# Kernel optimization log

Measured on AMD Instinct MI355X. Metric: run time of the kernel, lower is better.

## Reference

```python
import jax, jax.numpy as jnp
import numpy as np

B, S, D = 4, 2048, 256
H = 8
HD = D // H
FF = 1024
LEN_M1 = 513


def _layer_norm(x, gamma, beta, eps=1e-5):
    m = jnp.mean(x, axis=-1, keepdims=True)
    v = jnp.var(x, axis=-1, keepdims=True)
    return (x - m) * jax.lax.rsqrt(v + eps) * gamma + beta


def setup_inputs() -> dict:
    key = jax.random.key(0)
    ks = jax.random.split(key, 16)
    s = 0.02  # init scale for weights
    return {
        "src": jax.random.normal(ks[0], (B, S, D), dtype=jnp.float32),
        "Wq": jax.random.normal(ks[1], (D, D), dtype=jnp.float32) * s,
        "bq": jnp.zeros((D,), dtype=jnp.float32),
        "Wk": jax.random.normal(ks[2], (D, D), dtype=jnp.float32) * s,
        "bk": jnp.zeros((D,), dtype=jnp.float32),
        "Wv": jax.random.normal(ks[3], (D, D), dtype=jnp.float32) * s,
        "bv": jnp.zeros((D,), dtype=jnp.float32),
        "Wo": jax.random.normal(ks[4], (D, D), dtype=jnp.float32) * s,
        "bo": jnp.zeros((D,), dtype=jnp.float32),
        "W1": jax.random.normal(ks[5], (FF, D), dtype=jnp.float32) * s,
        "b1": jnp.zeros((FF,), dtype=jnp.float32),
        "W2": jax.random.normal(ks[6], (D, FF), dtype=jnp.float32) * s,
        "b2": jnp.zeros((D,), dtype=jnp.float32),
        "g1": jnp.ones((D,), dtype=jnp.float32),
        "be1": jnp.zeros((D,), dtype=jnp.float32),
        "g2": jnp.ones((D,), dtype=jnp.float32),
        "be2": jnp.zeros((D,), dtype=jnp.float32),
        "len_m1": LEN_M1,
    }


def reference(src, Wq, bq, Wk, bk, Wv, bv, Wo, bo, W1, b1, W2, b2, g1, be1, g2, be2, len_m1):
    Bb, Ss, Dd = src.shape
    hd = Dd // H
    # projections (torch Linear: x @ W.T + b), split heads -> [B,H,S,hd]
    q = (src @ Wq.T + bq).reshape(Bb, Ss, H, hd).transpose(0, 2, 1, 3)
    k = (src @ Wk.T + bk).reshape(Bb, Ss, H, hd).transpose(0, 2, 1, 3)
    v = (src @ Wv.T + bv).reshape(Bb, Ss, H, hd).transpose(0, 2, 1, 3)
    scores = jnp.einsum("bhqd,bhkd->bhqk", q, k) / np.sqrt(hd).astype(np.float32)
    # causal mask + global prefix block: masked where j > i OR (i < len_m1 and j >= len_m1)
    i = jnp.arange(Ss)[:, None]
    j = jnp.arange(Ss)[None, :]
    mask = (j > i) | ((i < len_m1) & (j >= len_m1))
    scores = jnp.where(mask, -jnp.inf, scores)
    attn = jax.nn.softmax(scores, axis=-1)
    ao = jnp.einsum("bhqk,bhkd->bhqd", attn, v).transpose(0, 2, 1, 3).reshape(Bb, Ss, Dd)
    src2 = _layer_norm(src + (ao @ Wo.T + bo), g1, be1)
    ff = jax.nn.gelu(src2 @ W1.T + b1, approximate=False) @ W2.T + b2
    return _layer_norm(src2 + ff, g2, be2)
```

## Files before the change

kernel.cpp:

```cpp
#include <hip/hip_runtime.h>
#include <math.h>

#define NB 4
#define NS 2048
#define ND 256
#define NH 8
#define NHD 32
#define NFF 1024
#define NM (NB*NS)
#define KPAD 40
#define VSP 72
#define VTP 72
#define AS 264
#define QSCALE 0.2550181657f

typedef __attribute__((ext_vector_type(4))) short short4v;
typedef __attribute__((ext_vector_type(8))) short short8v;
typedef __attribute__((ext_vector_type(4))) float f32x4;
typedef unsigned short us;

__device__ __forceinline__ us f2bf(float f){
  union { float f; unsigned u; } c; c.f = f;
  unsigned u = c.u + 0x7fffu + ((c.u >> 16) & 1u);
  return (us)(u >> 16);
}

__device__ __forceinline__ float wsum(float v){
  #pragma unroll
  for(int o=32;o>0;o>>=1) v += __shfl_xor(v,o);
  return v;
}

__global__ __launch_bounds__(256) void prep_kernel(
    const float* __restrict__ src,
    const float* __restrict__ Wq, const float* __restrict__ Wk, const float* __restrict__ Wv,
    const float* __restrict__ Wo, const float* __restrict__ W1, const float* __restrict__ W2,
    const float* __restrict__ bq,
    us* __restrict__ X, us* __restrict__ Wqkvb, us* __restrict__ Wob,
    us* __restrict__ W1b, us* __restrict__ W2b, float* __restrict__ bqs){
  unsigned bid = blockIdx.x;
  if (bid == 1408){ bqs[threadIdx.x] = bq[threadIdx.x]*QSCALE; return; }
  unsigned u = bid*256u + threadIdx.x;
  const float* sp; us* dp; float sc = 1.f;
  if (u < 262144u){ sp = src + (size_t)u*8; dp = X + (size_t)u*8; }
  else {
    unsigned v = u - 262144u;
    if      (v <  8192u){ sp = Wq + (size_t)v*8;            dp = Wqkvb + (size_t)v*8;            sc = QSCALE; }
    else if (v < 16384u){ sp = Wk + (size_t)(v- 8192u)*8;   dp = Wqkvb + 65536 + (size_t)(v- 8192u)*8; }
    else if (v < 24576u){ sp = Wv + (size_t)(v-16384u)*8;   dp = Wqkvb + 131072 + (size_t)(v-16384u)*8; }
    else if (v < 32768u){ sp = Wo + (size_t)(v-24576u)*8;   dp = Wob + (size_t)(v-24576u)*8; }
    else if (v < 65536u){ sp = W1 + (size_t)(v-32768u)*8;   dp = W1b + (size_t)(v-32768u)*8; }
    else               { sp = W2 + (size_t)(v-65536u)*8;    dp = W2b + (size_t)(v-65536u)*8; }
  }
  float4 a = *(const float4*)sp, b = *(const float4*)(sp+4);
  short8v o;
  o[0]=(short)f2bf(a.x*sc); o[1]=(short)f2bf(a.y*sc); o[2]=(short)f2bf(a.z*sc); o[3]=(short)f2bf(a.w*sc);
  o[4]=(short)f2bf(b.x*sc); o[5]=(short)f2bf(b.y*sc); o[6]=(short)f2bf(b.z*sc); o[7]=(short)f2bf(b.w*sc);
  *(short8v*)dp = o;
}

template<int KTOT, int EPI>
__global__ __launch_bounds__(256) void gemm_kernel(
    const us* __restrict__ A, const us* __restrict__ W,
    const float* __restrict__ bias0, const float* __restrict__ bias1, const float* __restrict__ bias2,
    us* __restrict__ outb, us* __restrict__ outv){
  __shared__ us Asl[64*AS];
  const int t = threadIdx.x, l = t&63, wv = t>>6;
  const int lx = l&15, lw = l>>4;
  const int m0 = blockIdx.y*64;
  const int n0 = blockIdx.x*128 + wv*32;

  f32x4 acc[4][2];
  #pragma unroll
  for(int mb=0;mb<4;mb++)
    #pragma unroll
    for(int nb=0;nb<2;nb++) acc[mb][nb] = (f32x4){0.f,0.f,0.f,0.f};

  for (int kc = 0; kc < KTOT; kc += 256){
    __syncthreads();
    #pragma unroll
    for (int it=0; it<8; it++){
      int idx = it*256 + t;
      int r = idx>>5, c = idx&31;
      *(short8v*)&Asl[r*AS + c*8] = *(const short8v*)(A + (size_t)(m0+r)*KTOT + kc + c*8);
    }
    __syncthreads();
    short8v bf[2][8];
    #pragma unroll
    for (int nb=0; nb<2; nb++)
      #pragma unroll
      for (int ks=0; ks<8; ks++)
        bf[nb][ks] = *(const short8v*)(W + (size_t)(n0 + nb*16 + lx)*KTOT + kc + ks*32 + 8*lw);
    #pragma unroll
    for (int ks=0; ks<8; ks++){
      short8v af[4];
      #pragma unroll
      for (int mb=0; mb<4; mb++)
        af[mb] = *(const short8v*)&Asl[(mb*16+lx)*AS + ks*32 + 8*lw];
      #pragma unroll
      for (int mb=0; mb<4; mb++){
        acc[mb][0] = __builtin_amdgcn_mfma_f32_16x16x32_bf16(af[mb], bf[0][ks], acc[mb][0], 0,0,0);
        acc[mb][1] = __builtin_amdgcn_mfma_f32_16x16x32_bf16(af[mb], bf[1][ks], acc[mb][1], 0,0,0);
      }
    }
  }
  const int mr0 = m0 + 4*lw;
  #pragma unroll
  for (int nb=0; nb<2; nb++){
    int n = n0 + nb*16 + lx;
    if (EPI == 0){
      int seg = n >> 8, nn = n & 255;
      const float* bp = (seg==0) ? bias0 : (seg==1) ? bias1 : bias2;
      float bb = bp[nn];
      if (seg < 2){
        us* op = outb + (size_t)seg*((size_t)NM*ND) + nn;
        #pragma unroll
        for (int mb=0; mb<4; mb++)
          #pragma unroll
          for (int r=0; r<4; r++)
            op[(size_t)(mr0 + mb*16 + r)*ND] = f2bf(acc[mb][nb][r] + bb);
      } else {
        int hh = nn >> 5, dd = nn & 31;
        int bidx = mr0 >> 11;
        int s0 = mr0 & 2047;
        us* vp = outv + (((size_t)bidx*NH + hh)*NHD + dd)*NS;
        #pragma unroll
        for (int mb=0; mb<4; mb++){
          short4v v4;
          #pragma unroll
          for (int r=0; r<4; r++) v4[r] = (short)f2bf(acc[mb][nb][r] + bb);
          *(short4v*)(vp + s0 + mb*16) = v4;
        }
      }
    } else {
      float bb = bias0[n];
      #pragma unroll
      for (int mb=0; mb<4; mb++)
        #pragma unroll
        for (int r=0; r<4; r++){
          float x = acc[mb][nb][r] + bb;
          float g = 0.5f*x*(1.f + erff(x*0.70710678118654752f));
          outb[(size_t)(mr0 + mb*16 + r)*NFF + n] = f2bf(g);
        }
    }
  }
}

template<int KTOT>
__global__ __launch_bounds__(256) void gemm2_kernel(
    const us* __restrict__ A, const us* __restrict__ W,
    const float* __restrict__ bias, const float* __restrict__ resid,
    float* __restrict__ outf){
  __shared__ us Asl[32*AS];
  const int t = threadIdx.x, l = t&63, wv = t>>6;
  const int lx = l&15, lw = l>>4;
  const int m0 = blockIdx.y*32;
  const int n0 = blockIdx.x*128 + wv*32;

  f32x4 acc[2][2];
  #pragma unroll
  for(int mb=0;mb<2;mb++)
    #pragma unroll
    for(int nb=0;nb<2;nb++) acc[mb][nb] = (f32x4){0.f,0.f,0.f,0.f};

  for (int kc = 0; kc < KTOT; kc += 256){
    __syncthreads();
    #pragma unroll
    for (int it=0; it<4; it++){
      int idx = it*256 + t;
      int r = idx>>5, c = idx&31;
      *(short8v*)&Asl[r*AS + c*8] = *(const short8v*)(A + (size_t)(m0+r)*KTOT + kc + c*8);
    }
    __syncthreads();
    short8v bf[2][8];
    #pragma unroll
    for (int nb=0; nb<2; nb++)
      #pragma unroll
      for (int ks=0; ks<8; ks++)
        bf[nb][ks] = *(const short8v*)(W + (size_t)(n0 + nb*16 + lx)*KTOT + kc + ks*32 + 8*lw);
    #pragma unroll
    for (int ks=0; ks<8; ks++){
      short8v af[2];
      #pragma unroll
      for (int mb=0; mb<2; mb++)
        af[mb] = *(const short8v*)&Asl[(mb*16+lx)*AS + ks*32 + 8*lw];
      #pragma unroll
      for (int mb=0; mb<2; mb++){
        acc[mb][0] = __builtin_amdgcn_mfma_f32_16x16x32_bf16(af[mb], bf[0][ks], acc[mb][0], 0,0,0);
        acc[mb][1] = __builtin_amdgcn_mfma_f32_16x16x32_bf16(af[mb], bf[1][ks], acc[mb][1], 0,0,0);
      }
    }
  }
  const int mr0 = m0 + 4*lw;
  #pragma unroll
  for (int nb=0; nb<2; nb++){
    int n = n0 + nb*16 + lx;
    float bb = bias[n];
    #pragma unroll
    for (int mb=0; mb<2; mb++)
      #pragma unroll
      for (int r=0; r<4; r++){
        size_t off = (size_t)(mr0 + mb*16 + r)*ND + n;
        outf[off] = acc[mb][nb][r] + bb + resid[off];
      }
  }
}

__global__ __launch_bounds__(256) void ln_kernel(
    const float* __restrict__ Xin, const float* __restrict__ g, const float* __restrict__ be,
    us* __restrict__ outb, float* __restrict__ outf){
  const int t = threadIdx.x, lane = t&63, wv = t>>6;
  const int m0 = blockIdx.x*16;
  #pragma unroll
  for(int rr=0; rr<4; rr++){
    int r = m0 + wv*4 + rr;
    const float* xr = Xin + (size_t)r*ND;
    float x[4]; float s=0.f,q=0.f;
    #pragma unroll
    for(int k=0;k<4;k++){ x[k]=xr[lane+64*k]; s+=x[k]; q+=x[k]*x[k]; }
    s = wsum(s); q = wsum(q);
    float mean = s*(1.f/ND), var = q*(1.f/ND)-mean*mean;
    float rstd = rsqrtf(var+1e-5f);
    #pragma unroll
    for(int k=0;k<4;k++){
      int col = lane+64*k;
      float y = (x[k]-mean)*rstd*g[col] + be[col];
      if (outf) outf[(size_t)r*ND+col] = y;
      if (outb) outb[(size_t)r*ND+col] = f2bf(y);
    }
  }
}

template<bool MASK>
__device__ __forceinline__ void attn_tile(
    const us* __restrict__ Kl, const us* __restrict__ Vl,
    const short8v qf, const int lx, const int lw, const int jt, const int qg,
    f32x4& acc0, f32x4& acc1, float& lsum){
  f32x4 s4[4];
  #pragma unroll
  for (int kb=0; kb<4; kb++){
    short8v kf = *(const short8v*)(Kl + (kb*16 + lx)*KPAD + 8*lw);
    f32x4 z = {0.f,0.f,0.f,0.f};
    s4[kb] = __builtin_amdgcn_mfma_f32_16x16x32_bf16(kf, qf, z, 0,0,0);
  }
  float p[16];
  #pragma unroll
  for (int kb=0; kb<4; kb++)
    #pragma unroll
    for (int r=0; r<4; r++){
      float x = exp2f(s4[kb][r]);
      if (MASK) x = ((jt + 16*kb + 4*lw + r) > qg) ? 0.f : x;
      p[kb*4+r] = x;
    }
  {
    float a0=p[0]+p[1],   a1=p[2]+p[3],   a2=p[4]+p[5],   a3=p[6]+p[7];
    float a4=p[8]+p[9],   a5=p[10]+p[11], a6=p[12]+p[13], a7=p[14]+p[15];
    float b0=a0+a1, b1=a2+a3, b2=a4+a5, b3=a6+a7;
    lsum += (b0+b1) + (b2+b3);
  }
  #pragma unroll
  for (int c=0; c<2; c++){
    unsigned w0,w1,w2,w3;
    asm("v_cvt_pk_bf16_f32 %0, %1, %2" : "=v"(w0) : "v"(p[8*c+0]), "v"(p[8*c+1]));
    asm("v_cvt_pk_bf16_f32 %0, %1, %2" : "=v"(w1) : "v"(p[8*c+2]), "v"(p[8*c+3]));
    asm("v_cvt_pk_bf16_f32 %0, %1, %2" : "=v"(w2) : "v"(p[8*c+4]), "v"(p[8*c+5]));
    asm("v_cvt_pk_bf16_f32 %0, %1, %2" : "=v"(w3) : "v"(p[8*c+6]), "v"(p[8*c+7]));
    union { unsigned u[4]; short8v v; } pu;
    pu.u[0]=w0; pu.u[1]=w1; pu.u[2]=w2; pu.u[3]=w3;
    short8v pf = pu.v;
    short8v aL = *(const short8v*)(Vl + (size_t)( lx    )*VSP + 32*c + 8*lw);
    short8v aH = *(const short8v*)(Vl + (size_t)(16+lx  )*VSP + 32*c + 8*lw);
    acc0 = __builtin_amdgcn_mfma_f32_16x16x32_bf16(aL, pf, acc0, 0,0,0);
    acc1 = __builtin_amdgcn_mfma_f32_16x16x32_bf16(aH, pf, acc1, 0,0,0);
  }
}

__global__ __launch_bounds__(256) void attn_kernel(
    const us* __restrict__ Q, const us* __restrict__ K,
    const us* __restrict__ Vt, us* __restrict__ AO){
  __shared__ us Klds[2][64*KPAD];
  __shared__ us Vs[2][32*VSP];
  __shared__ us Ex[4][16*VTP];

  const int t = threadIdx.x, l = t & 63, wv = t >> 6;
  const int lx = l & 15, lw = l >> 4;
  const int bid = blockIdx.x;
  const int qtile = 31 - (bid >> 5);
  const int bh = bid & 31;
  const int b = bh >> 3, h = bh & 7;
  const int qbase = qtile*64 + wv*16;
  const int qg = qbase + lx;

  const us* Qg = Q + ((size_t)b*NS)*ND + h*NHD;
  const us* Kg = K + ((size_t)b*NS)*ND + h*NHD;
  const us* Vg = Vt + (size_t)bh*NHD*NS;

  short8v qf = *(const short8v*)(Qg + (size_t)(qbase + lx)*ND + 8*lw);

  f32x4 acc0 = {0.f,0.f,0.f,0.f}, acc1 = {0.f,0.f,0.f,0.f};
  float lsum = 0.f;

  const int kr = t >> 2, kp = t & 3;
  const int vd = t >> 3, vp = t & 7;
  const int vS0 = 32*(vp>>2) + 16*(vp&1) + 4*((vp>>1)&1);
  const int jmax = qtile*64;

  {
    short8v k0 = *(const short8v*)(Kg + (size_t)kr*ND + kp*8);
    short8v v0 = *(const short8v*)(Vg + (size_t)vd*NS + vp*8);
    *(short8v*)&Klds[0][kr*KPAD + kp*8] = k0;
    short4v lo = {v0[0],v0[1],v0[2],v0[3]}, hi = {v0[4],v0[5],v0[6],v0[7]};
    *(short4v*)&Vs[0][vd*VSP + vS0]     = lo;
    *(short4v*)&Vs[0][vd*VSP + vS0 + 8] = hi;
  }
  __syncthreads();

  int cur = 0;
  for (int jt = 0; jt < jmax; jt += 64){
    short8v kn = *(const short8v*)(Kg + (size_t)(jt + 64 + kr)*ND + kp*8);
    short8v vn = *(const short8v*)(Vg + (size_t)vd*NS + (jt + 64) + vp*8);
    attn_tile<false>(&Klds[cur][0], &Vs[cur][0], qf, lx, lw, jt, qg, acc0, acc1, lsum);
    *(short8v*)&Klds[cur^1][kr*KPAD + kp*8] = kn;
    short4v lo = {vn[0],vn[1],vn[2],vn[3]}, hi = {vn[4],vn[5],vn[6],vn[7]};
    *(short4v*)&Vs[cur^1][vd*VSP + vS0]     = lo;
    *(short4v*)&Vs[cur^1][vd*VSP + vS0 + 8] = hi;
    __syncthreads();
    cur ^= 1;
  }
  attn_tile<true>(&Klds[cur][0], &Vs[cur][0], qf, lx, lw, jmax, qg, acc0, acc1, lsum);

  float lt = lsum + __shfl_xor(lsum, 16);
  lt += __shfl_xor(lt, 32);
  float inv = 1.f / lt;
  float* ol = (float*)&Ex[wv][0];
  #pragma unroll
  for (int r=0;r<4;r++){
    ol[lx*36 +      4*lw + r] = acc0[r]*inv;
    ol[lx*36 + 16 + 4*lw + r] = acc1[r]*inv;
  }
  int rr = l >> 2, cc = l & 3;
  const float* op8 = &ol[rr*36 + cc*8];
  short8v o8;
  #pragma unroll
  for (int j=0;j<8;j++) o8[j] = (short)f2bf(op8[j]);
  *(short8v*)(AO + ((size_t)(b*NS + qbase + rr))*ND + h*NHD + cc*8) = o8;
}

extern "C" void kernel_launch(void* const* d_in, const int* in_sizes, int n_in,
                              void* d_out, int out_size, void* d_ws, size_t ws_size,
                              hipStream_t stream){
  const float* src = (const float*)d_in[0];
  const float* Wq  = (const float*)d_in[1];
  const float* bq  = (const float*)d_in[2];
  const float* Wk  = (const float*)d_in[3];
  const float* bk  = (const float*)d_in[4];
  const float* Wv  = (const float*)d_in[5];
  const float* bv  = (const float*)d_in[6];
  const float* Wo  = (const float*)d_in[7];
  const float* bo  = (const float*)d_in[8];
  const float* W1  = (const float*)d_in[9];
  const float* b1  = (const float*)d_in[10];
  const float* W2  = (const float*)d_in[11];
  const float* b2  = (const float*)d_in[12];
  const float* g1  = (const float*)d_in[13];
  const float* be1 = (const float*)d_in[14];
  const float* g2  = (const float*)d_in[15];
  const float* be2 = (const float*)d_in[16];

  const size_t MB = 1048576;
  unsigned char* w8 = (unsigned char*)d_ws;
  us* X     = (us*)(w8 + 0);
  us* Qb    = (us*)(w8 + 4*MB);
  us* Kb    = (us*)(w8 + 8*MB);
  us* Vtg   = (us*)(w8 + 12*MB);
  us* AO    = (us*)(w8 + 16*MB);
  us* S2b   = (us*)(w8 + 20*MB);
  us* FF    = (us*)(w8 + 24*MB);
  us* Wqkvb = (us*)(w8 + 40*MB);
  us* Wob   = (us*)(w8 + 40*MB + 384*1024);
  us* W1b   = (us*)(w8 + 40*MB + 512*1024);
  us* W2b   = (us*)(w8 + 40*MB + 1024*1024);
  float* bqs   = (float*)(w8 + 40*MB + 1536*1024);
  float* S2pre = (float*)(w8 + 42*MB);
  float* S2f   = (float*)(w8 + 50*MB);
  float* Ypre  = (float*)(w8 + 0);
  float* out = (float*)d_out;

  prep_kernel<<<1409, 256, 0, stream>>>(src, Wq,Wk,Wv,Wo,W1,W2, bq,
                                        X, Wqkvb, Wob, W1b, W2b, bqs);
  gemm_kernel<256,0><<<dim3(6,128), 256, 0, stream>>>(X, Wqkvb, bqs, bk, bv, Qb, Vtg);
  attn_kernel<<<1024, 256, 0, stream>>>(Qb, Kb, Vtg, AO);
  gemm2_kernel<256><<<dim3(2,256), 256, 0, stream>>>(AO, Wob, bo, src, S2pre);
  ln_kernel<<<NM/16, 256, 0, stream>>>(S2pre, g1, be1, S2b, S2f);
  gemm_kernel<256,2><<<dim3(8,128), 256, 0, stream>>>(S2b, W1b, b1, nullptr, nullptr, FF, nullptr);
  gemm2_kernel<1024><<<dim3(2,256), 256, 0, stream>>>(FF, W2b, b2, S2f, Ypre);
  ln_kernel<<<NM/16, 256, 0, stream>>>(Ypre, g2, be2, nullptr, out);
}
```

Measured before the change: 111.0 us.

## Fuse input conversion into QKV GEMM and LayerNorm1 into FFN1 GEMM

```diff
diff --git a/kernel.cpp b/kernel.cpp
--- a/kernel.cpp
+++ b/kernel.cpp
@@ -24,6 +24,9 @@
   unsigned u = c.u + 0x7fffu + ((c.u >> 16) & 1u);
   return (us)(u >> 16);
 }
+__device__ __forceinline__ float bf2f(us u){
+  union { unsigned u; float f; } c; c.u = ((unsigned)u) << 16; return c.f;
+}
 
 __device__ __forceinline__ float wsum(float v){
   #pragma unroll
@@ -32,26 +35,21 @@
 }
 
 __global__ __launch_bounds__(256) void prep_kernel(
-    const float* __restrict__ src,
     const float* __restrict__ Wq, const float* __restrict__ Wk, const float* __restrict__ Wv,
     const float* __restrict__ Wo, const float* __restrict__ W1, const float* __restrict__ W2,
     const float* __restrict__ bq,
-    us* __restrict__ X, us* __restrict__ Wqkvb, us* __restrict__ Wob,
+    us* __restrict__ Wqkvb, us* __restrict__ Wob,
     us* __restrict__ W1b, us* __restrict__ W2b, float* __restrict__ bqs){
   unsigned bid = blockIdx.x;
-  if (bid == 1408){ bqs[threadIdx.x] = bq[threadIdx.x]*QSCALE; return; }
-  unsigned u = bid*256u + threadIdx.x;
+  if (bid == 384){ bqs[threadIdx.x] = bq[threadIdx.x]*QSCALE; return; }
+  unsigned v = bid*256u + threadIdx.x;
   const float* sp; us* dp; float sc = 1.f;
-  if (u < 262144u){ sp = src + (size_t)u*8; dp = X + (size_t)u*8; }
-  else {
-    unsigned v = u - 262144u;
-    if      (v <  8192u){ sp = Wq + (size_t)v*8;            dp = Wqkvb + (size_t)v*8;            sc = QSCALE; }
-    else if (v < 16384u){ sp = Wk + (size_t)(v- 8192u)*8;   dp = Wqkvb + 65536 + (size_t)(v- 8192u)*8; }
-    else if (v < 24576u){ sp = Wv + (size_t)(v-16384u)*8;   dp = Wqkvb + 131072 + (size_t)(v-16384u)*8; }
-    else if (v < 32768u){ sp = Wo + (size_t)(v-24576u)*8;   dp = Wob + (size_t)(v-24576u)*8; }
-    else if (v < 65536u){ sp = W1 + (size_t)(v-32768u)*8;   dp = W1b + (size_t)(v-32768u)*8; }
-    else               { sp = W2 + (size_t)(v-65536u)*8;    dp = W2b + (size_t)(v-65536u)*8; }
-  }
+  if      (v <  8192u){ sp = Wq + (size_t)v*8;            dp = Wqkvb + (size_t)v*8;            sc = QSCALE; }
+  else if (v < 16384u){ sp = Wk + (size_t)(v- 8192u)*8;   dp = Wqkvb + 65536 + (size_t)(v- 8192u)*8; }
+  else if (v < 24576u){ sp = Wv + (size_t)(v-16384u)*8;   dp = Wqkvb + 131072 + (size_t)(v-16384u)*8; }
+  else if (v < 32768u){ sp = Wo + (size_t)(v-24576u)*8;   dp = Wob + (size_t)(v-24576u)*8; }
+  else if (v < 65536u){ sp = W1 + (size_t)(v-32768u)*8;   dp = W1b + (size_t)(v-32768u)*8; }
+  else               { sp = W2 + (size_t)(v-65536u)*8;    dp = W2b + (size_t)(v-65536u)*8; }
   float4 a = *(const float4*)sp, b = *(const float4*)(sp+4);
   short8v o;
   o[0]=(short)f2bf(a.x*sc); o[1]=(short)f2bf(a.y*sc); o[2]=(short)f2bf(a.z*sc); o[3]=(short)f2bf(a.w*sc);
@@ -59,11 +57,13 @@
   *(short8v*)dp = o;
 }
 
-template<int KTOT, int EPI>
+template<int KTOT, int EPI, int AF32>
 __global__ __launch_bounds__(256) void gemm_kernel(
-    const us* __restrict__ A, const us* __restrict__ W,
+    const us* __restrict__ A, const float* __restrict__ Af,
+    const us* __restrict__ W,
     const float* __restrict__ bias0, const float* __restrict__ bias1, const float* __restrict__ bias2,
-    us* __restrict__ outb, us* __restrict__ outv){
+    const float* __restrict__ resid, const us* __restrict__ residb,
+    us* __restrict__ outb, us* __restrict__ outv, float* __restrict__ outf){
   __shared__ us Asl[64*AS];
   const int t = threadIdx.x, l = t&63, wv = t>>6;
   const int lx = l&15, lw = l>>4;
@@ -78,11 +78,22 @@
 
   for (int kc = 0; kc < KTOT; kc += 256){
     __syncthreads();
-    #pragma unroll
-    for (int it=0; it<8; it++){
-      int idx = it*256 + t;
-      int r = idx>>5, c = idx&31;
-      *(short8v*)&Asl[r*AS + c*8] = *(const short8v*)(A + (size_t)(m0+r)*KTOT + kc + c*8);
+    if (AF32){
+      #pragma unroll
+      for (int it=0; it<16; it++){
+        int idx = it*256 + t;
+        int r = idx>>6, c = idx&63;
+        float4 v = *(const float4*)(Af + (size_t)(m0+r)*KTOT + kc + c*4);
+        short4v o4 = { (short)f2bf(v.x),(short)f2bf(v.y),(short)f2bf(v.z),(short)f2bf(v.w) };
+        *(short4v*)&Asl[r*AS + c*4] = o4;
+      }
+    } else {
+      #pragma unroll
+      for (int it=0; it<8; it++){
+        int idx = it*256 + t;
+        int r = idx>>5, c = idx&31;
+        *(short8v*)&Asl[r*AS + c*8] = *(const short8v*)(A + (size_t)(m0+r)*KTOT + kc + c*8);
+      }
     }
     __syncthreads();
     short8v bf[2][8];
@@ -132,6 +143,24 @@
           *(short4v*)(vp + s0 + mb*16) = v4;
         }
       }
+    } else if (EPI == 1){
+      float bb = bias0[n];
+      #pragma unroll
+      for (int mb=0; mb<4; mb++)
+        #pragma unroll
+        for (int r=0; r<4; r++){
+          size_t off = (size_t)(mr0 + mb*16 + r)*ND + n;
+          outf[off] = acc[mb][nb][r] + bb + resid[off];
+        }
+    } else if (EPI == 3){
+      float bb = bias0[n];
+      #pragma unroll
+      for (int mb=0; mb<4; mb++)
+        #pragma unroll
+        for (int r=0; r<4; r++){
+          size_t off = (size_t)(mr0 + mb*16 + r)*ND + n;
+          outf[off] = acc[mb][nb][r] + bb + bf2f(residb[off]);
+        }
     } else {
       float bb = bias0[n];
       #pragma unroll
@@ -146,49 +175,58 @@
   }
 }
 
-template<int KTOT>
-__global__ __launch_bounds__(256) void gemm2_kernel(
-    const us* __restrict__ A, const us* __restrict__ W,
-    const float* __restrict__ bias, const float* __restrict__ resid,
-    float* __restrict__ outf){
-  __shared__ us Asl[32*AS];
+__global__ __launch_bounds__(256) void ffn1_ln_kernel(
+    const float* __restrict__ S2pre, const float* __restrict__ g, const float* __restrict__ be,
+    const us* __restrict__ W, const float* __restrict__ bias,
+    us* __restrict__ S2b, us* __restrict__ FF){
+  __shared__ us Asl[64*AS];
   const int t = threadIdx.x, l = t&63, wv = t>>6;
   const int lx = l&15, lw = l>>4;
-  const int m0 = blockIdx.y*32;
+  const int m0 = blockIdx.y*64;
   const int n0 = blockIdx.x*128 + wv*32;
 
-  f32x4 acc[2][2];
-  #pragma unroll
-  for(int mb=0;mb<2;mb++)
+  #pragma unroll
+  for (int rr=0; rr<16; rr++){
+    int rl = wv*16 + rr;
+    const float* xr = S2pre + (size_t)(m0+rl)*ND;
+    float x[4]; float s=0.f,q=0.f;
+    #pragma unroll
+    for (int k=0;k<4;k++){ x[k]=xr[l+64*k]; s+=x[k]; q+=x[k]*x[k]; }
+    s = wsum(s); q = wsum(q);
+    float mean = s*(1.f/ND), var = q*(1.f/ND)-mean*mean;
+    float rstd = rsqrtf(var+1e-5f);
+    #pragma unroll
+    for (int k=0;k<4;k++){
+      int col = l+64*k;
+      us y = f2bf((x[k]-mean)*rstd*g[col] + be[col]);
+      Asl[rl*AS + col] = y;
+      S2b[(size_t)(m0+rl)*ND + col] = y;
+    }
+  }
+  __syncthreads();
+
+  f32x4 acc[4][2];
+  #pragma unroll
+  for(int mb=0;mb<4;mb++)
     #pragma unroll
     for(int nb=0;nb<2;nb++) acc[mb][nb] = (f32x4){0.f,0.f,0.f,0.f};
 
-  for (int kc = 0; kc < KTOT; kc += 256){
-    __syncthreads();
-    #pragma unroll
-    for (int it=0; it<4; it++){
-      int idx = it*256 + t;
-      int r = idx>>5, c = idx&31;
-      *(short8v*)&Asl[r*AS + c*8] = *(const short8v*)(A + (size_t)(m0+r)*KTOT + kc + c*8);
-    }
-    __syncthreads();
-    short8v bf[2][8];
-    #pragma unroll
-    for (int nb=0; nb<2; nb++)
-      #pragma unroll
-      for (int ks=0; ks<8; ks++)
-        bf[nb][ks] = *(const short8v*)(W + (size_t)(n0 + nb*16 + lx)*KTOT + kc + ks*32 + 8*lw);
-    #pragma unroll
-    for (int ks=0; ks<8; ks++){
-      short8v af[2];
-      #pragma unroll
-      for (int mb=0; mb<2; mb++)
-        af[mb] = *(const short8v*)&Asl[(mb*16+lx)*AS + ks*32 + 8*lw];
-      #pragma unroll
-      for (int mb=0; mb<2; mb++){
-        acc[mb][0] = __builtin_amdgcn_mfma_f32_16x16x32_bf16(af[mb], bf[0][ks], acc[mb][0], 0,0,0);
-        acc[mb][1] = __builtin_amdgcn_mfma_f32_16x16x32_bf16(af[mb], bf[1][ks], acc[mb][1], 0,0,0);
-      }
+  short8v bf[2][8];
+  #pragma unroll
+  for (int nb=0; nb<2; nb++)
+    #pragma unroll
+    for (int ks=0; ks<8; ks++)
+      bf[nb][ks] = *(const short8v*)(W + (size_t)(n0 + nb*16 + lx)*ND + ks*32 + 8*lw);
+  #pragma unroll
+  for (int ks=0; ks<8; ks++){
+    short8v af[4];
+    #pragma unroll
+    for (int mb=0; mb<4; mb++)
+      af[mb] = *(const short8v*)&Asl[(mb*16+lx)*AS + ks*32 + 8*lw];
+    #pragma unroll
+    for (int mb=0; mb<4; mb++){
+      acc[mb][0] = __builtin_amdgcn_mfma_f32_16x16x32_bf16(af[mb], bf[0][ks], acc[mb][0], 0,0,0);
+      acc[mb][1] = __builtin_amdgcn_mfma_f32_16x16x32_bf16(af[mb], bf[1][ks], acc[mb][1], 0,0,0);
     }
   }
   const int mr0 = m0 + 4*lw;
@@ -197,18 +235,19 @@
     int n = n0 + nb*16 + lx;
     float bb = bias[n];
     #pragma unroll
-    for (int mb=0; mb<2; mb++)
+    for (int mb=0; mb<4; mb++)
       #pragma unroll
       for (int r=0; r<4; r++){
-        size_t off = (size_t)(mr0 + mb*16 + r)*ND + n;
-        outf[off] = acc[mb][nb][r] + bb + resid[off];
+        float x = acc[mb][nb][r] + bb;
+        float gl = 0.5f*x*(1.f + erff(x*0.70710678118654752f));
+        FF[(size_t)(mr0 + mb*16 + r)*NFF + n] = f2bf(gl);
       }
   }
 }
 
 __global__ __launch_bounds__(256) void ln_kernel(
     const float* __restrict__ Xin, const float* __restrict__ g, const float* __restrict__ be,
-    us* __restrict__ outb, float* __restrict__ outf){
+    float* __restrict__ outf){
   const int t = threadIdx.x, lane = t&63, wv = t>>6;
   const int m0 = blockIdx.x*16;
   #pragma unroll
@@ -224,9 +263,7 @@
     #pragma unroll
     for(int k=0;k<4;k++){
       int col = lane+64*k;
-      float y = (x[k]-mean)*rstd*g[col] + be[col];
-      if (outf) outf[(size_t)r*ND+col] = y;
-      if (outb) outb[(size_t)r*ND+col] = f2bf(y);
+      outf[(size_t)r*ND+col] = (x[k]-mean)*rstd*g[col] + be[col];
     }
   }
 }
@@ -369,7 +406,6 @@
 
   const size_t MB = 1048576;
   unsigned char* w8 = (unsigned char*)d_ws;
-  us* X     = (us*)(w8 + 0);
   us* Qb    = (us*)(w8 + 4*MB);
   us* Kb    = (us*)(w8 + 8*MB);
   us* Vtg   = (us*)(w8 + 12*MB);
@@ -382,17 +418,16 @@
   us* W2b   = (us*)(w8 + 40*MB + 1024*1024);
   float* bqs   = (float*)(w8 + 40*MB + 1536*1024);
   float* S2pre = (float*)(w8 + 42*MB);
-  float* S2f   = (float*)(w8 + 50*MB);
   float* Ypre  = (float*)(w8 + 0);
+  Ypre = (float*)(w8 + 50*MB);
   float* out = (float*)d_out;
 
-  prep_kernel<<<1409, 256, 0, stream>>>(src, Wq,Wk,Wv,Wo,W1,W2, bq,
-                                        X, Wqkvb, Wob, W1b, W2b, bqs);
-  gemm_kernel<256,0><<<dim3(6,128), 256, 0, stream>>>(X, Wqkvb, bqs, bk, bv, Qb, Vtg);
+  prep_kernel<<<385, 256, 0, stream>>>(Wq,Wk,Wv,Wo,W1,W2, bq,
+                                       Wqkvb, Wob, W1b, W2b, bqs);
+  gemm_kernel<256,0,1><<<dim3(6,128), 256, 0, stream>>>(nullptr, src, Wqkvb, bqs, bk, bv, nullptr, nullptr, Qb, Vtg, nullptr);
   attn_kernel<<<1024, 256, 0, stream>>>(Qb, Kb, Vtg, AO);
-  gemm2_kernel<256><<<dim3(2,256), 256, 0, stream>>>(AO, Wob, bo, src, S2pre);
-  ln_kernel<<<NM/16, 256, 0, stream>>>(S2pre, g1, be1, S2b, S2f);
-  gemm_kernel<256,2><<<dim3(8,128), 256, 0, stream>>>(S2b, W1b, b1, nullptr, nullptr, FF, nullptr);
-  gemm2_kernel<1024><<<dim3(2,256), 256, 0, stream>>>(FF, W2b, b2, S2f, Ypre);
-  ln_kernel<<<NM/16, 256, 0, stream>>>(Ypre, g2, be2, nullptr, out);
-}
+  gemm_kernel<256,1,0><<<dim3(2,128), 256, 0, stream>>>(AO, nullptr, Wob, bo, nullptr, nullptr, src, nullptr, nullptr, nullptr, S2pre);
+  ffn1_ln_kernel<<<dim3(8,128), 256, 0, stream>>>(S2pre, g1, be1, W1b, b1, S2b, FF);
+  gemm_kernel<1024,3,0><<<dim3(2,128), 256, 0, stream>>>(FF, nullptr, W2b, b2, nullptr, nullptr, nullptr, S2b, nullptr, nullptr, Ypre);
+  ln_kernel<<<NM/16, 256, 0, stream>>>(Ypre, g2, be2, out);
+}
```

After: 110.6 us. Within noise of the previous version (-0.4%).
